# Performance work log

Measured on AMD Instinct MI355X. Metric: run time of the kernel, lower is better.

## Reference

```python
import jax, jax.numpy as jnp
import numpy as np


def _bilinear_sample(img, y, x):
    # img: [B,C,H,W]; y, x: [B,Gh,Gw] float sampling coords (pixel units)
    B, C, H, W = img.shape
    y0 = jnp.floor(y)
    x0 = jnp.floor(x)
    wy1 = y - y0
    wx1 = x - x0
    wy0 = 1.0 - wy1
    wx0 = 1.0 - wx1
    flat = img.reshape(B, C, H * W)

    def gather(yi, xi):
        valid = (yi >= 0) & (yi <= H - 1) & (xi >= 0) & (xi <= W - 1)
        yc = jnp.clip(yi, 0, H - 1).astype(jnp.int32)
        xc = jnp.clip(xi, 0, W - 1).astype(jnp.int32)
        idx = (yc * W + xc).reshape(B, 1, -1)  # [B,1,Gh*Gw]
        g = jnp.take_along_axis(flat, jnp.broadcast_to(idx, (B, C, idx.shape[-1])), axis=2)
        g = g.reshape(B, C, yi.shape[1], yi.shape[2])
        return g * valid[:, None].astype(img.dtype)

    out = (gather(y0, x0) * (wy0 * wx0)[:, None]
           + gather(y0, x0 + 1) * (wy0 * wx1)[:, None]
           + gather(y0 + 1, x0) * (wy1 * wx0)[:, None]
           + gather(y0 + 1, x0 + 1) * (wy1 * wx1)[:, None])
    return out


def setup_inputs() -> dict:
    key = jax.random.key(0)
    k1, k2 = jax.random.split(key)
    B, C, H, W = 32, 64, 128, 128
    Gh, Gw = 64, 64
    x = jax.random.normal(k1, (B, C, H, W), dtype=jnp.float32)
    offset = jax.random.normal(k2, (B, 2, Gh, Gw), dtype=jnp.float32)
    return {"x": x, "offset": offset, "grid_h": Gh, "grid_w": Gw, "shift": 0}


def reference(x, offset, grid_h, grid_w, shift):
    # Deformable feature-map resampling: sample input at a regular grid of
    # size (grid_h, grid_w) scaled to the input extent, shifted by `shift`,
    # displaced by learned per-location offsets (dy, dx), bilinear interp,
    # zeros outside bounds. Output: [B, C, grid_h, grid_w].
    B, C, H, W = x.shape
    scale_h = H / grid_h
    scale_w = W / grid_w
    gy = jnp.arange(grid_h, dtype=x.dtype) * scale_h + shift  # [Gh]
    gx = jnp.arange(grid_w, dtype=x.dtype) * scale_w + shift  # [Gw]
    y = gy[None, :, None] + offset[:, 0]  # [B,Gh,Gw]
    xx = gx[None, None, :] + offset[:, 1]  # [B,Gh,Gw]
    return _bilinear_sample(x, y, xx)
```

## Files before the change

kernel.cpp:

```cpp
#include <hip/hip_runtime.h>

#define BB 32
#define CC 64
#define HH 128
#define WW 128
#define GH 64
#define GW 64
#define PLANE (HH * WW)
#define OUTP  (GH * GW)

__global__ __launch_bounds__(1024) void defem_kernel(
    const float* __restrict__ x,
    const float* __restrict__ off,
    const int* __restrict__ shift_p,
    float* __restrict__ out)
{
    __shared__ float plane[PLANE];

    const int tid = threadIdx.x;
    const int blk = blockIdx.x;
    const int b   = blk >> 6;

    const float* __restrict__ src  = x + (size_t)blk * PLANE;
    const float* __restrict__ offb = off + (size_t)b * 2 * OUTP;

    #pragma unroll
    for (int k = 0; k < 4; ++k) {
        const int i = (k * 1024 + tid) * 4;
        *(float4*)(plane + i) = *(const float4*)(src + i);
    }

    float dys[4], dxs[4];
    #pragma unroll
    for (int k = 0; k < 4; ++k) {
        const int s = k * 1024 + tid;
        dys[k] = offb[s];
        dxs[k] = offb[OUTP + s];
    }
    const float shift = (float)shift_p[0];

    __syncthreads();

    float* __restrict__ obase = out + (size_t)blk * OUTP;

    #pragma unroll
    for (int k = 0; k < 4; ++k) {
        const int s  = k * 1024 + tid;
        const int gw = s & (GW - 1);
        const int gh = s >> 6;

        const float y  = (float)gh * 2.0f + shift + dys[k];
        const float xx = (float)gw * 2.0f + shift + dxs[k];

        const float y0f = floorf(y);
        const float x0f = floorf(xx);
        const float wy1 = y - y0f;
        const float wx1 = xx - x0f;
        const float wy0 = 1.0f - wy1;
        const float wx0 = 1.0f - wx1;
        const int y0 = (int)y0f;
        const int x0 = (int)x0f;
        const int y1 = y0 + 1;
        const int x1 = x0 + 1;

        const float vy0 = (y0 >= 0 && y0 < HH) ? 1.0f : 0.0f;
        const float vy1 = (y1 >= 0 && y1 < HH) ? 1.0f : 0.0f;
        const float vx0 = (x0 >= 0 && x0 < WW) ? 1.0f : 0.0f;
        const float vx1 = (x1 >= 0 && x1 < WW) ? 1.0f : 0.0f;

        const float w00 = wy0 * wx0 * vy0 * vx0;
        const float w01 = wy0 * wx1 * vy0 * vx1;
        const float w10 = wy1 * wx0 * vy1 * vx0;
        const float w11 = wy1 * wx1 * vy1 * vx1;

        const int yc0 = min(max(y0, 0), HH - 1);
        const int yc1 = min(max(y1, 0), HH - 1);
        const int xs  = min(max(x0, 0), WW - 2);
        const bool sel = (x0 == xs);

        const float u0a = sel ? w00 : w01;
        const float u0b = sel ? w01 : w00;
        const float u1a = sel ? w10 : w11;
        const float u1b = sel ? w11 : w10;

        const int rA = yc0 * WW + xs;
        const int rB = yc1 * WW + xs;

        const float a0 = plane[rA];
        const float a1 = plane[rA + 1];
        const float b0 = plane[rB];
        const float b1 = plane[rB + 1];

        obase[s] = a0 * u0a + a1 * u0b + b0 * u1a + b1 * u1b;
    }
}

extern "C" void kernel_launch(void* const* d_in, const int* in_sizes, int n_in,
                              void* d_out, int out_size, void* d_ws, size_t ws_size,
                              hipStream_t stream) {
    const float* x   = (const float*)d_in[0];
    const float* off = (const float*)d_in[1];
    const int* shift_p = (const int*)d_in[4];
    float* out = (float*)d_out;

    const int grid = BB * CC;
    defem_kernel<<<grid, 1024, 0, stream>>>(x, off, shift_p, out);
}
```

Before: 30.80 us.

## Process four channels per block with double-buffered async LDS plane staging

Each block now handles four channels of one batch. Bilinear indices and weights are computed once and reused across those channels. Input planes are staged with global_load_lds into two LDS buffers, so the load of the next plane overlaps the sampling of the current one. In exchange, LDS use doubles to 128KB per block and the grid shrinks by four, which lowers occupancy and the number of blocks in flight for a kernel that is largely bandwidth-bound.

```diff
diff --git a/kernel.cpp b/kernel.cpp
--- a/kernel.cpp
+++ b/kernel.cpp
@@ -8,6 +8,19 @@
 #define GW 64
 #define PLANE (HH * WW)
 #define OUTP  (GH * GW)
+#define CPB 4
+
+__device__ __forceinline__ void stage_plane(const float* __restrict__ src,
+                                            float* dst, int tid) {
+    #pragma unroll
+    for (int k = 0; k < 4; ++k) {
+        const int fo = k * 4096 + tid * 4;
+        __builtin_amdgcn_global_load_lds(
+            (const __attribute__((address_space(1))) void*)(src + fo),
+            (__attribute__((address_space(3))) void*)(dst + fo),
+            16, 0, 0);
+    }
+}
 
 __global__ __launch_bounds__(1024) void defem_kernel(
     const float* __restrict__ x,
@@ -15,33 +28,22 @@
     const int* __restrict__ shift_p,
     float* __restrict__ out)
 {
-    __shared__ float plane[PLANE];
+    __shared__ float lds[2 * PLANE];
 
     const int tid = threadIdx.x;
     const int blk = blockIdx.x;
-    const int b   = blk >> 6;
+    const int b   = blk >> 4;
+    const int c0  = (blk & 15) * CPB;
 
-    const float* __restrict__ src  = x + (size_t)blk * PLANE;
+    const float* __restrict__ src0 = x + (size_t)(b * CC + c0) * PLANE;
     const float* __restrict__ offb = off + (size_t)b * 2 * OUTP;
+    float* __restrict__ out0 = out + (size_t)(b * CC + c0) * OUTP;
 
-    #pragma unroll
-    for (int k = 0; k < 4; ++k) {
-        const int i = (k * 1024 + tid) * 4;
-        *(float4*)(plane + i) = *(const float4*)(src + i);
-    }
+    stage_plane(src0, lds, tid);
 
-    float dys[4], dxs[4];
-    #pragma unroll
-    for (int k = 0; k < 4; ++k) {
-        const int s = k * 1024 + tid;
-        dys[k] = offb[s];
-        dxs[k] = offb[OUTP + s];
-    }
     const float shift = (float)shift_p[0];
-
-    __syncthreads();
-
-    float* __restrict__ obase = out + (size_t)blk * OUTP;
+    int rA[4], rB[4];
+    float u0a[4], u0b[4], u1a[4], u1b[4];
 
     #pragma unroll
     for (int k = 0; k < 4; ++k) {
@@ -49,8 +51,11 @@
         const int gw = s & (GW - 1);
         const int gh = s >> 6;
 
-        const float y  = (float)gh * 2.0f + shift + dys[k];
-        const float xx = (float)gw * 2.0f + shift + dxs[k];
+        const float dy = offb[s];
+        const float dx = offb[OUTP + s];
+
+        const float y  = (float)gh * 2.0f + shift + dy;
+        const float xx = (float)gw * 2.0f + shift + dx;
 
         const float y0f = floorf(y);
         const float x0f = floorf(xx);
@@ -78,20 +83,36 @@
         const int xs  = min(max(x0, 0), WW - 2);
         const bool sel = (x0 == xs);
 
-        const float u0a = sel ? w00 : w01;
-        const float u0b = sel ? w01 : w00;
-        const float u1a = sel ? w10 : w11;
-        const float u1b = sel ? w11 : w10;
+        u0a[k] = sel ? w00 : w01;
+        u0b[k] = sel ? w01 : w00;
+        u1a[k] = sel ? w10 : w11;
+        u1b[k] = sel ? w11 : w10;
+        rA[k] = yc0 * WW + xs;
+        rB[k] = yc1 * WW + xs;
+    }
 
-        const int rA = yc0 * WW + xs;
-        const int rB = yc1 * WW + xs;
+    __syncthreads();
 
-        const float a0 = plane[rA];
-        const float a1 = plane[rA + 1];
-        const float b0 = plane[rB];
-        const float b1 = plane[rB + 1];
+    #pragma unroll
+    for (int p = 0; p < CPB; ++p) {
+        if (p + 1 < CPB)
+            stage_plane(src0 + (size_t)(p + 1) * PLANE,
+                        lds + ((p + 1) & 1) * PLANE, tid);
 
-        obase[s] = a0 * u0a + a1 * u0b + b0 * u1a + b1 * u1b;
+        const float* __restrict__ pl = lds + (p & 1) * PLANE;
+        float* __restrict__ ob = out0 + (size_t)p * OUTP;
+
+        #pragma unroll
+        for (int k = 0; k < 4; ++k) {
+            const int s = k * 1024 + tid;
+            const float a0 = pl[rA[k]];
+            const float a1 = pl[rA[k] + 1];
+            const float b0 = pl[rB[k]];
+            const float b1 = pl[rB[k] + 1];
+            ob[s] = a0 * u0a[k] + a1 * u0b[k] + b0 * u1a[k] + b1 * u1b[k];
+        }
+
+        __syncthreads();
     }
 }
 
@@ -103,6 +124,6 @@
     const int* shift_p = (const int*)d_in[4];
     float* out = (float*)d_out;
 
-    const int grid = BB * CC;
+    const int grid = BB * CC / CPB;
     defem_kernel<<<grid, 1024, 0, stream>>>(x, off, shift_p, out);
 }
```

After: 33.41 us. 8.5% more time.
